# Kernel tuning notes

Measured on AMD Instinct MI355X. Metric: run time of the kernel, lower is better.

## Reference

```python
import jax, jax.numpy as jnp
import numpy as np

DIM = 192
WIN = 8
HEADS = 6
HEAD_DIM = DIM // HEADS
SCALE = HEAD_DIM ** -0.5
N = WIN * WIN


def _relative_position_index():
    coords = np.stack(np.meshgrid(np.arange(WIN), np.arange(WIN), indexing='ij'))  # [2,W,W]
    flat = coords.reshape(2, -1)  # [2,N]
    rel = flat[:, :, None] - flat[:, None, :]  # [2,N,N]
    rel = rel.transpose(1, 2, 0)
    rel[:, :, 0] += WIN - 1
    rel[:, :, 1] += WIN - 1
    rel[:, :, 0] *= 2 * WIN - 1
    return rel.sum(-1).astype(np.int32)  # [N,N]


def setup_inputs() -> dict:
    key = jax.random.key(0)
    ks = jax.random.split(key, 6)
    B = 4096
    x = jax.random.normal(ks[0], (B, N, DIM), dtype=jnp.float32)
    qkv_w = jax.random.normal(ks[1], (3 * DIM, DIM), dtype=jnp.float32) * (DIM ** -0.5)
    qkv_b = jnp.zeros((3 * DIM,), dtype=jnp.float32)
    proj_w = jax.random.normal(ks[2], (DIM, DIM), dtype=jnp.float32) * (DIM ** -0.5)
    proj_b = jnp.zeros((DIM,), dtype=jnp.float32)
    num_rel = (2 * WIN - 1) * (2 * WIN - 1)
    bias_table = jax.random.normal(ks[3], (num_rel, HEADS), dtype=jnp.float32) * 0.02
    rel_idx = jnp.asarray(_relative_position_index())
    return {"x": x, "qkv_w": qkv_w, "qkv_b": qkv_b, "proj_w": proj_w,
            "proj_b": proj_b, "bias_table": bias_table, "rel_idx": rel_idx}


def reference(x, qkv_w, qkv_b, proj_w, proj_b, bias_table, rel_idx):
    B, n, C = x.shape
    qkv = x @ qkv_w.T + qkv_b  # [B,N,3C]
    qkv = qkv.reshape(B, n, 3, HEADS, HEAD_DIM).transpose(2, 0, 3, 1, 4)  # [3,B,H,N,hd]
    q, k, v = qkv[0], qkv[1], qkv[2]
    attn = jnp.einsum('bhnd,bhmd->bhnm', q * SCALE, k)  # [B,H,N,N]
    bias = bias_table[rel_idx]  # [N,N,H]
    attn = attn + bias.transpose(2, 0, 1)[None]  # add [1,H,N,N]
    attn = jax.nn.softmax(attn, axis=-1)
    out = jnp.einsum('bhnm,bhmd->bhnd', attn, v)
    out = out.transpose(0, 2, 1, 3).reshape(B, n, C)
    return out @ proj_w.T + proj_b
```

## Files before the change

### kernel.cpp

```cpp
#include <hip/hip_runtime.h>

#define NTOK 64
#define DIM 192
#define HEADS 6
#define HD 32
#define SCALE 0.17677669529663687f
#define LOG2E 1.4426950408889634f
#define XSS 200

typedef __bf16 bf16x8 __attribute__((ext_vector_type(8)));
typedef __bf16 bf16x4 __attribute__((ext_vector_type(4)));
typedef float f32x4 __attribute__((ext_vector_type(4)));

union F4 { float4 v; float f[4]; };

__global__ void prep_kernel(const float* __restrict__ qkv_w,
                            const float* __restrict__ proj_w,
                            const float* __restrict__ bias_table,
                            const int* __restrict__ rel_idx,
                            unsigned short* __restrict__ wq,
                            unsigned short* __restrict__ wp,
                            float* __restrict__ biasf) {
  int i = blockIdx.x * 256 + threadIdx.x;
  if (i < 3 * DIM * DIM) ((__bf16*)wq)[i] = (__bf16)qkv_w[i];
  if (i < DIM * DIM) ((__bf16*)wp)[i] = (__bf16)proj_w[i];
  if (i < HEADS * NTOK * NTOK) {
    int h = i >> 12;
    int nm = i & 4095;
    biasf[i] = bias_table[rel_idx[nm] * HEADS + h] * LOG2E;
  }
}

__global__ __launch_bounds__(384) void attn_kernel(
    const float* __restrict__ x,
    const float* __restrict__ qkv_b,
    const float* __restrict__ proj_b,
    const unsigned short* __restrict__ wq,
    const unsigned short* __restrict__ wp,
    const float* __restrict__ biasf,
    float* __restrict__ out) {
  __shared__ unsigned short xs[NTOK * XSS];

  const int tid = threadIdx.x;
  const int w = tid >> 6;
  const int lane = tid & 63;
  const int l15 = lane & 15;
  const int quad = lane >> 4;
  const long b = blockIdx.x;
  const int h = w;

  {
    const float4* xg = (const float4*)(x + b * (NTOK * DIM));
    #pragma unroll
    for (int it = 0; it < 8; ++it) {
      int idx = tid + it * 384;
      float4 v = xg[idx];
      int row = idx / 48;
      int col = (idx % 48) * 4;
      bf16x4 o;
      o[0] = (__bf16)v.x; o[1] = (__bf16)v.y;
      o[2] = (__bf16)v.z; o[3] = (__bf16)v.w;
      *(bf16x4*)&xs[row * XSS + col] = o;
    }
  }
  __syncthreads();

  const int prm = ((l15 >> 2) << 3) | (l15 & 3);
  const f32x4 zero = {0.f, 0.f, 0.f, 0.f};
  const float qsc = SCALE * LOG2E;

  bf16x8 qfrag[4];
  {
    const unsigned short* wqh = wq + ((size_t)h * 32) * DIM;
    F4 qb0, qb1;
    qb0.v = *(const float4*)(qkv_b + h * 32 + quad * 8);
    qb1.v = *(const float4*)(qkv_b + h * 32 + quad * 8 + 4);
    float qb0s[4], qb1s[4];
    #pragma unroll
    for (int g = 0; g < 4; ++g) { qb0s[g] = qb0.f[g] * qsc; qb1s[g] = qb1.f[g] * qsc; }
    #pragma unroll
    for (int nt = 0; nt < 4; ++nt) {
      bf16x8 xn[6];
      #pragma unroll
      for (int ks = 0; ks < 6; ++ks)
        xn[ks] = *(const bf16x8*)&xs[(nt * 16 + l15) * XSS + ks * 32 + quad * 8];
      f32x4 a0 = zero, a1 = zero;
      #pragma unroll
      for (int ks = 0; ks < 6; ++ks) {
        bf16x8 w0 = *(const bf16x8*)(wqh + (size_t)(prm + 0) * DIM + ks * 32 + quad * 8);
        bf16x8 w1 = *(const bf16x8*)(wqh + (size_t)(prm + 4) * DIM + ks * 32 + quad * 8);
        a0 = __builtin_amdgcn_mfma_f32_16x16x32_bf16(w0, xn[ks], a0, 0, 0, 0);
        a1 = __builtin_amdgcn_mfma_f32_16x16x32_bf16(w1, xn[ks], a1, 0, 0, 0);
      }
      bf16x8 t;
      #pragma unroll
      for (int g = 0; g < 4; ++g) {
        t[g]     = (__bf16)fmaf(a0[g], qsc, qb0s[g]);
        t[4 + g] = (__bf16)fmaf(a1[g], qsc, qb1s[g]);
      }
      qfrag[nt] = t;
    }
  }

  bf16x8 kfrag[4];
  bf16x8 vbu[2][2];
  {
    const unsigned short* wkh = wq + ((size_t)(192 + h * 32)) * DIM;
    const unsigned short* wvh = wq + ((size_t)(384 + h * 32)) * DIM;
    F4 kb0, kb1;
    kb0.v = *(const float4*)(qkv_b + 192 + h * 32 + quad * 8);
    kb1.v = *(const float4*)(qkv_b + 192 + h * 32 + quad * 8 + 4);
    const float vbias0 = qkv_b[384 + h * 32 + l15];
    const float vbias1 = qkv_b[384 + h * 32 + 16 + l15];
    #pragma unroll
    for (int mt = 0; mt < 4; ++mt) {
      const int kv = mt >> 1, half = mt & 1;
      const int xrow = kv * 32 + half * 4 + prm;
      bf16x8 xp[6];
      #pragma unroll
      for (int ks = 0; ks < 6; ++ks)
        xp[ks] = *(const bf16x8*)&xs[xrow * XSS + ks * 32 + quad * 8];
      f32x4 ka0 = zero, ka1 = zero, va0 = zero, va1 = zero;
      #pragma unroll
      for (int ks = 0; ks < 6; ++ks) {
        bf16x8 wk0 = *(const bf16x8*)(wkh + (size_t)(prm + 0) * DIM + ks * 32 + quad * 8);
        bf16x8 wk1 = *(const bf16x8*)(wkh + (size_t)(prm + 4) * DIM + ks * 32 + quad * 8);
        bf16x8 wv0 = *(const bf16x8*)(wvh + (size_t)(l15 + 0) * DIM + ks * 32 + quad * 8);
        bf16x8 wv1 = *(const bf16x8*)(wvh + (size_t)(l15 + 16) * DIM + ks * 32 + quad * 8);
        ka0 = __builtin_amdgcn_mfma_f32_16x16x32_bf16(wk0, xp[ks], ka0, 0, 0, 0);
        ka1 = __builtin_amdgcn_mfma_f32_16x16x32_bf16(wk1, xp[ks], ka1, 0, 0, 0);
        va0 = __builtin_amdgcn_mfma_f32_16x16x32_bf16(xp[ks], wv0, va0, 0, 0, 0);
        va1 = __builtin_amdgcn_mfma_f32_16x16x32_bf16(xp[ks], wv1, va1, 0, 0, 0);
      }
      bf16x8 t;
      #pragma unroll
      for (int g = 0; g < 4; ++g) {
        t[g]     = (__bf16)(ka0[g] + kb0.f[g]);
        t[4 + g] = (__bf16)(ka1[g] + kb1.f[g]);
        vbu[0][kv][half * 4 + g] = (__bf16)(va0[g] + vbias0);
        vbu[1][kv][half * 4 + g] = (__bf16)(va1[g] + vbias1);
      }
      kfrag[mt] = t;
    }
  }

  const float* bh = biasf + h * 4096;
  f32x4 s[4][4];
  #pragma unroll
  for (int mt = 0; mt < 4; ++mt)
    #pragma unroll
    for (int nt = 0; nt < 4; ++nt) {
      f32x4 binit = *(const f32x4*)(bh + (nt * 16 + l15) * 64 +
                                    (mt >> 1) * 32 + quad * 8 + (mt & 1) * 4);
      s[mt][nt] = __builtin_amdgcn_mfma_f32_16x16x32_bf16(kfrag[mt], qfrag[nt], binit, 0, 0, 0);
    }

  bf16x8 pa[4][2];
  #pragma unroll
  for (int nt = 0; nt < 4; ++nt) {
    float p[16];
    #pragma unroll
    for (int t = 0; t < 16; ++t)
      p[t] = __builtin_amdgcn_exp2f(s[t >> 2][nt][t & 3]);
    float s0 = (p[0] + p[1]) + (p[2] + p[3]);
    float s1 = (p[4] + p[5]) + (p[6] + p[7]);
    float s2 = (p[8] + p[9]) + (p[10] + p[11]);
    float s3 = (p[12] + p[13]) + (p[14] + p[15]);
    float sm = (s0 + s1) + (s2 + s3);
    sm += __shfl_xor(sm, 16);
    sm += __shfl_xor(sm, 32);
    float r = __builtin_amdgcn_rcpf(sm);
    bf16x8 t0, t1;
    #pragma unroll
    for (int j = 0; j < 8; ++j) {
      t0[j] = (__bf16)(p[j] * r);
      t1[j] = (__bf16)(p[8 + j] * r);
    }
    pa[nt][0] = t0;
    pa[nt][1] = t1;
  }

  f32x4 o[4][2];
  #pragma unroll
  for (int nt = 0; nt < 4; ++nt)
    #pragma unroll
    for (int c2 = 0; c2 < 2; ++c2) {
      f32x4 acc = __builtin_amdgcn_mfma_f32_16x16x32_bf16(pa[nt][0], vbu[c2][0], zero, 0, 0, 0);
      o[nt][c2] = __builtin_amdgcn_mfma_f32_16x16x32_bf16(pa[nt][1], vbu[c2][1], acc, 0, 0, 0);
    }

  __syncthreads();
  #pragma unroll
  for (int nt = 0; nt < 4; ++nt)
    #pragma unroll
    for (int c2 = 0; c2 < 2; ++c2)
      #pragma unroll
      for (int g = 0; g < 4; ++g)
        *(__bf16*)&xs[(nt * 16 + quad * 4 + g) * XSS + h * 32 + c2 * 16 + l15] =
            (__bf16)o[nt][c2][g];
  __syncthreads();

  {
    bf16x8 af[4][6];
    #pragma unroll
    for (int nt = 0; nt < 4; ++nt)
      #pragma unroll
      for (int ks = 0; ks < 6; ++ks)
        af[nt][ks] = *(const bf16x8*)&xs[(nt * 16 + l15) * XSS + ks * 32 + quad * 8];
    float* og = out + b * (NTOK * DIM);
    #pragma unroll
    for (int i = 0; i < 2; ++i) {
      const int e = w * 32 + i * 16 + l15;
      f32x4 acc[4] = {zero, zero, zero, zero};
      #pragma unroll
      for (int ks = 0; ks < 6; ++ks) {
        bf16x8 bw = *(const bf16x8*)(wp + (size_t)e * DIM + ks * 32 + quad * 8);
        #pragma unroll
        for (int nt = 0; nt < 4; ++nt)
          acc[nt] = __builtin_amdgcn_mfma_f32_16x16x32_bf16(af[nt][ks], bw, acc[nt], 0, 0, 0);
      }
      const float pb = proj_b[e];
      #pragma unroll
      for (int nt = 0; nt < 4; ++nt)
        #pragma unroll
        for (int g = 0; g < 4; ++g)
          og[(nt * 16 + quad * 4 + g) * DIM + e] = acc[nt][g] + pb;
    }
  }
}

extern "C" void kernel_launch(void* const* d_in, const int* in_sizes, int n_in,
                              void* d_out, int out_size, void* d_ws, size_t ws_size,
                              hipStream_t stream) {
  const float* x          = (const float*)d_in[0];
  const float* qkv_w      = (const float*)d_in[1];
  const float* qkv_b      = (const float*)d_in[2];
  const float* proj_w     = (const float*)d_in[3];
  const float* proj_b     = (const float*)d_in[4];
  const float* bias_table = (const float*)d_in[5];
  const int*   rel_idx    = (const int*)d_in[6];

  unsigned short* wq = (unsigned short*)d_ws;
  unsigned short* wp = wq + 3 * DIM * DIM;
  float* biasf = (float*)(wp + DIM * DIM);

  prep_kernel<<<432, 256, 0, stream>>>(qkv_w, proj_w, bias_table, rel_idx, wq, wp, biasf);
  attn_kernel<<<4096, 384, 0, stream>>>(x, qkv_b, proj_b, wq, wp, biasf, (float*)d_out);
}
```

Measured before the change: 526.6 us.

## Process two attention windows per block to reuse weight fragments

Each block now handles two windows instead of one, so every global load of Q/K/V/proj weight fragments and bias values feeds MFMAs for both windows. The aim is to halve per-window weight and bias traffic from L2/global and amortise block setup, with the grid halved to 2048. In exchange, LDS use doubles and register pressure rises (two sets of q/k/v fragments and accumulators), which may reduce occupancy or cause spills.

```diff
diff --git a/kernel.cpp b/kernel.cpp
--- a/kernel.cpp
+++ b/kernel.cpp
@@ -39,28 +39,30 @@
     const unsigned short* __restrict__ wp,
     const float* __restrict__ biasf,
     float* __restrict__ out) {
-  __shared__ unsigned short xs[NTOK * XSS];
+  __shared__ unsigned short xs[2][NTOK * XSS];
 
   const int tid = threadIdx.x;
   const int w = tid >> 6;
   const int lane = tid & 63;
   const int l15 = lane & 15;
   const int quad = lane >> 4;
-  const long b = blockIdx.x;
+  const long b0 = (long)blockIdx.x * 2;
   const int h = w;
 
   {
-    const float4* xg = (const float4*)(x + b * (NTOK * DIM));
-    #pragma unroll
-    for (int it = 0; it < 8; ++it) {
+    const float4* xg = (const float4*)(x + b0 * (NTOK * DIM));
+    #pragma unroll
+    for (int it = 0; it < 16; ++it) {
+      int win = it >> 3;
       int idx = tid + it * 384;
+      int r = idx - win * 3072;
       float4 v = xg[idx];
-      int row = idx / 48;
-      int col = (idx % 48) * 4;
+      int row = r / 48;
+      int col = (r % 48) * 4;
       bf16x4 o;
       o[0] = (__bf16)v.x; o[1] = (__bf16)v.y;
       o[2] = (__bf16)v.z; o[3] = (__bf16)v.w;
-      *(bf16x4*)&xs[row * XSS + col] = o;
+      *(bf16x4*)&xs[win][row * XSS + col] = o;
     }
   }
   __syncthreads();
@@ -69,7 +71,7 @@
   const f32x4 zero = {0.f, 0.f, 0.f, 0.f};
   const float qsc = SCALE * LOG2E;
 
-  bf16x8 qfrag[4];
+  bf16x8 qfrag[2][4];
   {
     const unsigned short* wqh = wq + ((size_t)h * 32) * DIM;
     F4 qb0, qb1;
@@ -80,30 +82,33 @@
     for (int g = 0; g < 4; ++g) { qb0s[g] = qb0.f[g] * qsc; qb1s[g] = qb1.f[g] * qsc; }
     #pragma unroll
     for (int nt = 0; nt < 4; ++nt) {
-      bf16x8 xn[6];
-      #pragma unroll
-      for (int ks = 0; ks < 6; ++ks)
-        xn[ks] = *(const bf16x8*)&xs[(nt * 16 + l15) * XSS + ks * 32 + quad * 8];
-      f32x4 a0 = zero, a1 = zero;
+      f32x4 a0[2] = {zero, zero}, a1[2] = {zero, zero};
       #pragma unroll
       for (int ks = 0; ks < 6; ++ks) {
         bf16x8 w0 = *(const bf16x8*)(wqh + (size_t)(prm + 0) * DIM + ks * 32 + quad * 8);
         bf16x8 w1 = *(const bf16x8*)(wqh + (size_t)(prm + 4) * DIM + ks * 32 + quad * 8);
-        a0 = __builtin_amdgcn_mfma_f32_16x16x32_bf16(w0, xn[ks], a0, 0, 0, 0);
-        a1 = __builtin_amdgcn_mfma_f32_16x16x32_bf16(w1, xn[ks], a1, 0, 0, 0);
-      }
-      bf16x8 t;
-      #pragma unroll
-      for (int g = 0; g < 4; ++g) {
-        t[g]     = (__bf16)fmaf(a0[g], qsc, qb0s[g]);
-        t[4 + g] = (__bf16)fmaf(a1[g], qsc, qb1s[g]);
-      }
-      qfrag[nt] = t;
-    }
-  }
-
-  bf16x8 kfrag[4];
-  bf16x8 vbu[2][2];
+        #pragma unroll
+        for (int win = 0; win < 2; ++win) {
+          bf16x8 xn = *(const bf16x8*)&xs[win][(nt * 16 + l15) * XSS + ks * 32 + quad * 8];
+          a0[win] = __builtin_amdgcn_mfma_f32_16x16x32_bf16(w0, xn, a0[win], 0, 0, 0);
+          a1[win] = __builtin_amdgcn_mfma_f32_16x16x32_bf16(w1, xn, a1[win], 0, 0, 0);
+        }
+      }
+      #pragma unroll
+      for (int win = 0; win < 2; ++win) {
+        bf16x8 t;
+        #pragma unroll
+        for (int g = 0; g < 4; ++g) {
+          t[g]     = (__bf16)fmaf(a0[win][g], qsc, qb0s[g]);
+          t[4 + g] = (__bf16)fmaf(a1[win][g], qsc, qb1s[g]);
+        }
+        qfrag[win][nt] = t;
+      }
+    }
+  }
+
+  bf16x8 kfrag[2][4];
+  bf16x8 vbu[2][2][2];
   {
     const unsigned short* wkh = wq + ((size_t)(192 + h * 32)) * DIM;
     const unsigned short* wvh = wq + ((size_t)(384 + h * 32)) * DIM;
@@ -116,115 +121,127 @@
     for (int mt = 0; mt < 4; ++mt) {
       const int kv = mt >> 1, half = mt & 1;
       const int xrow = kv * 32 + half * 4 + prm;
-      bf16x8 xp[6];
-      #pragma unroll
-      for (int ks = 0; ks < 6; ++ks)
-        xp[ks] = *(const bf16x8*)&xs[xrow * XSS + ks * 32 + quad * 8];
-      f32x4 ka0 = zero, ka1 = zero, va0 = zero, va1 = zero;
+      f32x4 ka0[2] = {zero, zero}, ka1[2] = {zero, zero};
+      f32x4 va0[2] = {zero, zero}, va1[2] = {zero, zero};
       #pragma unroll
       for (int ks = 0; ks < 6; ++ks) {
         bf16x8 wk0 = *(const bf16x8*)(wkh + (size_t)(prm + 0) * DIM + ks * 32 + quad * 8);
         bf16x8 wk1 = *(const bf16x8*)(wkh + (size_t)(prm + 4) * DIM + ks * 32 + quad * 8);
         bf16x8 wv0 = *(const bf16x8*)(wvh + (size_t)(l15 + 0) * DIM + ks * 32 + quad * 8);
         bf16x8 wv1 = *(const bf16x8*)(wvh + (size_t)(l15 + 16) * DIM + ks * 32 + quad * 8);
-        ka0 = __builtin_amdgcn_mfma_f32_16x16x32_bf16(wk0, xp[ks], ka0, 0, 0, 0);
-        ka1 = __builtin_amdgcn_mfma_f32_16x16x32_bf16(wk1, xp[ks], ka1, 0, 0, 0);
-        va0 = __builtin_amdgcn_mfma_f32_16x16x32_bf16(xp[ks], wv0, va0, 0, 0, 0);
-        va1 = __builtin_amdgcn_mfma_f32_16x16x32_bf16(xp[ks], wv1, va1, 0, 0, 0);
-      }
-      bf16x8 t;
-      #pragma unroll
-      for (int g = 0; g < 4; ++g) {
-        t[g]     = (__bf16)(ka0[g] + kb0.f[g]);
-        t[4 + g] = (__bf16)(ka1[g] + kb1.f[g]);
-        vbu[0][kv][half * 4 + g] = (__bf16)(va0[g] + vbias0);
-        vbu[1][kv][half * 4 + g] = (__bf16)(va1[g] + vbias1);
-      }
-      kfrag[mt] = t;
+        #pragma unroll
+        for (int win = 0; win < 2; ++win) {
+          bf16x8 xp = *(const bf16x8*)&xs[win][xrow * XSS + ks * 32 + quad * 8];
+          ka0[win] = __builtin_amdgcn_mfma_f32_16x16x32_bf16(wk0, xp, ka0[win], 0, 0, 0);
+          ka1[win] = __builtin_amdgcn_mfma_f32_16x16x32_bf16(wk1, xp, ka1[win], 0, 0, 0);
+          va0[win] = __builtin_amdgcn_mfma_f32_16x16x32_bf16(xp, wv0, va0[win], 0, 0, 0);
+          va1[win] = __builtin_amdgcn_mfma_f32_16x16x32_bf16(xp, wv1, va1[win], 0, 0, 0);
+        }
+      }
+      #pragma unroll
+      for (int win = 0; win < 2; ++win) {
+        bf16x8 t;
+        #pragma unroll
+        for (int g = 0; g < 4; ++g) {
+          t[g]     = (__bf16)(ka0[win][g] + kb0.f[g]);
+          t[4 + g] = (__bf16)(ka1[win][g] + kb1.f[g]);
+          vbu[win][0][kv][half * 4 + g] = (__bf16)(va0[win][g] + vbias0);
+          vbu[win][1][kv][half * 4 + g] = (__bf16)(va1[win][g] + vbias1);
+        }
+        kfrag[win][mt] = t;
+      }
     }
   }
 
   const float* bh = biasf + h * 4096;
-  f32x4 s[4][4];
-  #pragma unroll
-  for (int mt = 0; mt < 4; ++mt)
-    #pragma unroll
-    for (int nt = 0; nt < 4; ++nt) {
-      f32x4 binit = *(const f32x4*)(bh + (nt * 16 + l15) * 64 +
-                                    (mt >> 1) * 32 + quad * 8 + (mt & 1) * 4);
-      s[mt][nt] = __builtin_amdgcn_mfma_f32_16x16x32_bf16(kfrag[mt], qfrag[nt], binit, 0, 0, 0);
-    }
-
-  bf16x8 pa[4][2];
+  bf16x8 pa[2][4][2];
   #pragma unroll
   for (int nt = 0; nt < 4; ++nt) {
-    float p[16];
-    #pragma unroll
-    for (int t = 0; t < 16; ++t)
-      p[t] = __builtin_amdgcn_exp2f(s[t >> 2][nt][t & 3]);
-    float s0 = (p[0] + p[1]) + (p[2] + p[3]);
-    float s1 = (p[4] + p[5]) + (p[6] + p[7]);
-    float s2 = (p[8] + p[9]) + (p[10] + p[11]);
-    float s3 = (p[12] + p[13]) + (p[14] + p[15]);
-    float sm = (s0 + s1) + (s2 + s3);
-    sm += __shfl_xor(sm, 16);
-    sm += __shfl_xor(sm, 32);
-    float r = __builtin_amdgcn_rcpf(sm);
-    bf16x8 t0, t1;
-    #pragma unroll
-    for (int j = 0; j < 8; ++j) {
-      t0[j] = (__bf16)(p[j] * r);
-      t1[j] = (__bf16)(p[8 + j] * r);
-    }
-    pa[nt][0] = t0;
-    pa[nt][1] = t1;
-  }
-
-  f32x4 o[4][2];
+    f32x4 binit[4];
+    #pragma unroll
+    for (int mt = 0; mt < 4; ++mt)
+      binit[mt] = *(const f32x4*)(bh + (nt * 16 + l15) * 64 +
+                                  (mt >> 1) * 32 + quad * 8 + (mt & 1) * 4);
+    #pragma unroll
+    for (int win = 0; win < 2; ++win) {
+      f32x4 sv[4];
+      #pragma unroll
+      for (int mt = 0; mt < 4; ++mt)
+        sv[mt] = __builtin_amdgcn_mfma_f32_16x16x32_bf16(kfrag[win][mt], qfrag[win][nt],
+                                                         binit[mt], 0, 0, 0);
+      float p[16];
+      #pragma unroll
+      for (int t = 0; t < 16; ++t)
+        p[t] = __builtin_amdgcn_exp2f(sv[t >> 2][t & 3]);
+      float s0 = (p[0] + p[1]) + (p[2] + p[3]);
+      float s1 = (p[4] + p[5]) + (p[6] + p[7]);
+      float s2 = (p[8] + p[9]) + (p[10] + p[11]);
+      float s3 = (p[12] + p[13]) + (p[14] + p[15]);
+      float sm = (s0 + s1) + (s2 + s3);
+      sm += __shfl_xor(sm, 16);
+      sm += __shfl_xor(sm, 32);
+      float r = __builtin_amdgcn_rcpf(sm);
+      bf16x8 t0, t1;
+      #pragma unroll
+      for (int j = 0; j < 8; ++j) {
+        t0[j] = (__bf16)(p[j] * r);
+        t1[j] = (__bf16)(p[8 + j] * r);
+      }
+      pa[win][nt][0] = t0;
+      pa[win][nt][1] = t1;
+    }
+  }
+
+  f32x4 o[2][4][2];
   #pragma unroll
   for (int nt = 0; nt < 4; ++nt)
     #pragma unroll
-    for (int c2 = 0; c2 < 2; ++c2) {
-      f32x4 acc = __builtin_amdgcn_mfma_f32_16x16x32_bf16(pa[nt][0], vbu[c2][0], zero, 0, 0, 0);
-      o[nt][c2] = __builtin_amdgcn_mfma_f32_16x16x32_bf16(pa[nt][1], vbu[c2][1], acc, 0, 0, 0);
-    }
+    for (int win = 0; win < 2; ++win)
+      #pragma unroll
+      for (int c2 = 0; c2 < 2; ++c2) {
+        f32x4 acc = __builtin_amdgcn_mfma_f32_16x16x32_bf16(pa[win][nt][0], vbu[win][c2][0],
+                                                            zero, 0, 0, 0);
+        o[win][nt][c2] = __builtin_amdgcn_mfma_f32_16x16x32_bf16(pa[win][nt][1], vbu[win][c2][1],
+                                                                 acc, 0, 0, 0);
+      }
 
   __syncthreads();
   #pragma unroll
-  for (int nt = 0; nt < 4; ++nt)
-    #pragma unroll
-    for (int c2 = 0; c2 < 2; ++c2)
-      #pragma unroll
-      for (int g = 0; g < 4; ++g)
-        *(__bf16*)&xs[(nt * 16 + quad * 4 + g) * XSS + h * 32 + c2 * 16 + l15] =
-            (__bf16)o[nt][c2][g];
+  for (int win = 0; win < 2; ++win)
+    #pragma unroll
+    for (int nt = 0; nt < 4; ++nt)
+      #pragma unroll
+      for (int c2 = 0; c2 < 2; ++c2)
+        #pragma unroll
+        for (int g = 0; g < 4; ++g)
+          *(__bf16*)&xs[win][(nt * 16 + quad * 4 + g) * XSS + h * 32 + c2 * 16 + l15] =
+              (__bf16)o[win][nt][c2][g];
   __syncthreads();
 
-  {
-    bf16x8 af[4][6];
-    #pragma unroll
-    for (int nt = 0; nt < 4; ++nt)
-      #pragma unroll
-      for (int ks = 0; ks < 6; ++ks)
-        af[nt][ks] = *(const bf16x8*)&xs[(nt * 16 + l15) * XSS + ks * 32 + quad * 8];
-    float* og = out + b * (NTOK * DIM);
-    #pragma unroll
-    for (int i = 0; i < 2; ++i) {
-      const int e = w * 32 + i * 16 + l15;
-      f32x4 acc[4] = {zero, zero, zero, zero};
-      #pragma unroll
-      for (int ks = 0; ks < 6; ++ks) {
-        bf16x8 bw = *(const bf16x8*)(wp + (size_t)e * DIM + ks * 32 + quad * 8);
-        #pragma unroll
-        for (int nt = 0; nt < 4; ++nt)
-          acc[nt] = __builtin_amdgcn_mfma_f32_16x16x32_bf16(af[nt][ks], bw, acc[nt], 0, 0, 0);
-      }
-      const float pb = proj_b[e];
+  #pragma unroll
+  for (int i = 0; i < 2; ++i) {
+    const int e = w * 32 + i * 16 + l15;
+    f32x4 acc[2][4] = {{zero, zero, zero, zero}, {zero, zero, zero, zero}};
+    #pragma unroll
+    for (int ks = 0; ks < 6; ++ks) {
+      bf16x8 bw = *(const bf16x8*)(wp + (size_t)e * DIM + ks * 32 + quad * 8);
+      #pragma unroll
+      for (int win = 0; win < 2; ++win)
+        #pragma unroll
+        for (int nt = 0; nt < 4; ++nt) {
+          bf16x8 a = *(const bf16x8*)&xs[win][(nt * 16 + l15) * XSS + ks * 32 + quad * 8];
+          acc[win][nt] = __builtin_amdgcn_mfma_f32_16x16x32_bf16(a, bw, acc[win][nt], 0, 0, 0);
+        }
+    }
+    const float pb = proj_b[e];
+    #pragma unroll
+    for (int win = 0; win < 2; ++win) {
+      float* og = out + (b0 + win) * (NTOK * DIM);
       #pragma unroll
       for (int nt = 0; nt < 4; ++nt)
         #pragma unroll
         for (int g = 0; g < 4; ++g)
-          og[(nt * 16 + quad * 4 + g) * DIM + e] = acc[nt][g] + pb;
+          og[(nt * 16 + quad * 4 + g) * DIM + e] = acc[win][nt][g] + pb;
     }
   }
 }
@@ -245,5 +262,5 @@
   float* biasf = (float*)(wp + DIM * DIM);
 
   prep_kernel<<<432, 256, 0, stream>>>(qkv_w, proj_w, bias_table, rel_idx, wq, wp, biasf);
-  attn_kernel<<<4096, 384, 0, stream>>>(x, qkv_b, proj_b, wq, wp, biasf, (float*)d_out);
+  attn_kernel<<<2048, 384, 0, stream>>>(x, qkv_b, proj_b, wq, wp, biasf, (float*)d_out);
 }
```

Measured after the change: 474.8 us. -9.8%, faster.

## Process two windows per block with 768 threads and fuse score into softmax loop

Applied to the files above, without the earlier changes.

Each block now handles two windows with 12 waves (head x window), doubling shared memory to two x tiles and halving the grid. The score MFMAs are moved inside the per-row softmax loop, so only four score accumulators are live at a time instead of sixteen, which lowers register pressure. The intent is better occupancy and amortized block overhead. The trade-offs are larger blocks, which may schedule less flexibly, and launch_bounds 768 capping registers per thread.

```diff
diff --git a/kernel.cpp b/kernel.cpp
--- a/kernel.cpp
+++ b/kernel.cpp
@@ -31,7 +31,7 @@
   }
 }
 
-__global__ __launch_bounds__(384) void attn_kernel(
+__global__ __launch_bounds__(768) void attn_kernel(
     const float* __restrict__ x,
     const float* __restrict__ qkv_b,
     const float* __restrict__ proj_b,
@@ -39,28 +39,30 @@
     const unsigned short* __restrict__ wp,
     const float* __restrict__ biasf,
     float* __restrict__ out) {
-  __shared__ unsigned short xs[NTOK * XSS];
+  __shared__ unsigned short xs[2][NTOK * XSS];
 
   const int tid = threadIdx.x;
   const int w = tid >> 6;
+  const int h = w >> 1;
+  const int win = w & 1;
   const int lane = tid & 63;
   const int l15 = lane & 15;
   const int quad = lane >> 4;
-  const long b = blockIdx.x;
-  const int h = w;
-
-  {
-    const float4* xg = (const float4*)(x + b * (NTOK * DIM));
+  const long b0 = (long)blockIdx.x * 2;
+
+  {
+    const float4* xg = (const float4*)(x + b0 * (NTOK * DIM));
     #pragma unroll
     for (int it = 0; it < 8; ++it) {
-      int idx = tid + it * 384;
-      float4 v = xg[idx];
-      int row = idx / 48;
-      int col = (idx % 48) * 4;
+      int wv = it >> 2;
+      int r = tid + (it & 3) * 768;
+      float4 v = xg[wv * 3072 + r];
+      int row = r / 48;
+      int col = (r % 48) * 4;
       bf16x4 o;
       o[0] = (__bf16)v.x; o[1] = (__bf16)v.y;
       o[2] = (__bf16)v.z; o[3] = (__bf16)v.w;
-      *(bf16x4*)&xs[row * XSS + col] = o;
+      *(bf16x4*)&xs[wv][row * XSS + col] = o;
     }
   }
   __syncthreads();
@@ -83,7 +85,7 @@
       bf16x8 xn[6];
       #pragma unroll
       for (int ks = 0; ks < 6; ++ks)
-        xn[ks] = *(const bf16x8*)&xs[(nt * 16 + l15) * XSS + ks * 32 + quad * 8];
+        xn[ks] = *(const bf16x8*)&xs[win][(nt * 16 + l15) * XSS + ks * 32 + quad * 8];
       f32x4 a0 = zero, a1 = zero;
       #pragma unroll
       for (int ks = 0; ks < 6; ++ks) {
@@ -119,7 +121,7 @@
       bf16x8 xp[6];
       #pragma unroll
       for (int ks = 0; ks < 6; ++ks)
-        xp[ks] = *(const bf16x8*)&xs[xrow * XSS + ks * 32 + quad * 8];
+        xp[ks] = *(const bf16x8*)&xs[win][xrow * XSS + ks * 32 + quad * 8];
       f32x4 ka0 = zero, ka1 = zero, va0 = zero, va1 = zero;
       #pragma unroll
       for (int ks = 0; ks < 6; ++ks) {
@@ -145,23 +147,20 @@
   }
 
   const float* bh = biasf + h * 4096;
-  f32x4 s[4][4];
-  #pragma unroll
-  for (int mt = 0; mt < 4; ++mt)
-    #pragma unroll
-    for (int nt = 0; nt < 4; ++nt) {
-      f32x4 binit = *(const f32x4*)(bh + (nt * 16 + l15) * 64 +
-                                    (mt >> 1) * 32 + quad * 8 + (mt & 1) * 4);
-      s[mt][nt] = __builtin_amdgcn_mfma_f32_16x16x32_bf16(kfrag[mt], qfrag[nt], binit, 0, 0, 0);
-    }
-
   bf16x8 pa[4][2];
   #pragma unroll
   for (int nt = 0; nt < 4; ++nt) {
+    f32x4 sv[4];
+    #pragma unroll
+    for (int mt = 0; mt < 4; ++mt) {
+      f32x4 binit = *(const f32x4*)(bh + (nt * 16 + l15) * 64 +
+                                    (mt >> 1) * 32 + quad * 8 + (mt & 1) * 4);
+      sv[mt] = __builtin_amdgcn_mfma_f32_16x16x32_bf16(kfrag[mt], qfrag[nt], binit, 0, 0, 0);
+    }
     float p[16];
     #pragma unroll
     for (int t = 0; t < 16; ++t)
-      p[t] = __builtin_amdgcn_exp2f(s[t >> 2][nt][t & 3]);
+      p[t] = __builtin_amdgcn_exp2f(sv[t >> 2][t & 3]);
     float s0 = (p[0] + p[1]) + (p[2] + p[3]);
     float s1 = (p[4] + p[5]) + (p[6] + p[7]);
     float s2 = (p[8] + p[9]) + (p[10] + p[11]);
@@ -196,7 +195,7 @@
     for (int c2 = 0; c2 < 2; ++c2)
       #pragma unroll
       for (int g = 0; g < 4; ++g)
-        *(__bf16*)&xs[(nt * 16 + quad * 4 + g) * XSS + h * 32 + c2 * 16 + l15] =
+        *(__bf16*)&xs[win][(nt * 16 + quad * 4 + g) * XSS + h * 32 + c2 * 16 + l15] =
             (__bf16)o[nt][c2][g];
   __syncthreads();
 
@@ -206,11 +205,11 @@
     for (int nt = 0; nt < 4; ++nt)
       #pragma unroll
       for (int ks = 0; ks < 6; ++ks)
-        af[nt][ks] = *(const bf16x8*)&xs[(nt * 16 + l15) * XSS + ks * 32 + quad * 8];
-    float* og = out + b * (NTOK * DIM);
+        af[nt][ks] = *(const bf16x8*)&xs[win][(nt * 16 + l15) * XSS + ks * 32 + quad * 8];
+    float* og = out + (b0 + win) * (NTOK * DIM);
     #pragma unroll
     for (int i = 0; i < 2; ++i) {
-      const int e = w * 32 + i * 16 + l15;
+      const int e = h * 32 + i * 16 + l15;
       f32x4 acc[4] = {zero, zero, zero, zero};
       #pragma unroll
       for (int ks = 0; ks < 6; ++ks) {
@@ -245,5 +244,5 @@
   float* biasf = (float*)(wp + DIM * DIM);
 
   prep_kernel<<<432, 256, 0, stream>>>(qkv_w, proj_w, bias_table, rel_idx, wq, wp, biasf);
-  attn_kernel<<<4096, 384, 0, stream>>>(x, qkv_b, proj_b, wq, wp, biasf, (float*)d_out);
+  attn_kernel<<<2048, 768, 0, stream>>>(x, qkv_b, proj_b, wq, wp, biasf, (float*)d_out);
 }
```

Result: no change. 535.4 us (+1.7%).
